# Kernel optimization log

Hardware: AMD Instinct MI355X
Metric: run time of the kernel (lower is better)

## Reference

```python
import jax, jax.numpy as jnp
import numpy as np

# Module hyperparameters (from init_kwargs)
N_HEAD = 16
D_K = 64
D_V = 64
TEMPERATURE = 0.7
TOP_K = 32
NEG_MIN = jnp.finfo(jnp.float32).min


def setup_inputs() -> dict:
    key = jax.random.key(0)
    ks = jax.random.split(key, 7)
    B, L, E = 2, 2048, 1024
    return {
        "q": jax.random.normal(ks[0], (B, L, E), jnp.float32),
        "k": jax.random.normal(ks[1], (B, L, E), jnp.float32),
        "v": jax.random.normal(ks[2], (B, L, D_V), jnp.float32),
        "w_q": jax.random.normal(ks[3], (N_HEAD * D_K, E), jnp.float32) * (E ** -0.5),
        "w_k": jax.random.normal(ks[4], (N_HEAD * D_K, E), jnp.float32) * (E ** -0.5),
        "w_v": jax.random.normal(ks[5], (N_HEAD * D_V, D_V), jnp.float32) * (D_V ** -0.5),
        "w_fc": jax.random.normal(ks[6], (D_V, N_HEAD * D_V), jnp.float32) * ((N_HEAD * D_V) ** -0.5),
    }


def _topk_restrict(logits):
    # Keep exactly TOP_K entries per row (scatter of top-k indices), fill rest with dtype min.
    B, H, Lq, Lk = logits.shape
    _, idx = jax.lax.top_k(logits, TOP_K)  # [B,H,Lq,TOP_K]
    bb = jnp.arange(B)[:, None, None, None]
    hh = jnp.arange(H)[None, :, None, None]
    qq = jnp.arange(Lq)[None, None, :, None]
    keep = jnp.zeros(logits.shape, bool).at[bb, hh, qq, idx].set(True)
    return jnp.where(keep, logits, NEG_MIN)


def reference(q, k, v, w_q, w_k, w_v, w_fc):
    B, Lq, _ = q.shape
    Lk = k.shape[1]
    Lv = v.shape[1]
    # Projections (bias-free linears), split heads: [B, H, L, d]
    q_proj = (q @ w_q.T).reshape(B, Lq, N_HEAD, D_K).transpose(0, 2, 1, 3)
    k_proj = (k @ w_k.T).reshape(B, Lk, N_HEAD, D_K).transpose(0, 2, 1, 3)
    v_proj = (v @ w_v.T).reshape(B, Lv, N_HEAD, D_V).transpose(0, 2, 1, 3)
    # Scaled QK^T in float32, then temperature scaling.
    logits = jnp.einsum("bhqd,bhkd->bhqk", q_proj / (D_K ** 0.5), k_proj).astype(jnp.float32)
    logits = logits / TEMPERATURE
    # Top-k restriction of attention logits (query_mask_flat=None -> applied to all queries).
    logits = _topk_restrict(logits)
    # Softmax selection; dropout is identity in eval / p=0.
    attn_probs = jax.nn.softmax(logits, axis=-1).astype(v.dtype)
    mixed = jnp.einsum("bhqk,bhkd->bhqd", attn_probs, v_proj)
    out = mixed.transpose(0, 2, 1, 3).reshape(B, Lq, N_HEAD * D_V)
    output = out @ w_fc.T
    return output, attn_probs
```

## Files before the change

### kernel.cpp

```cpp
#include <hip/hip_runtime.h>
#include <stdint.h>
#include <float.h>

constexpr int L = 2048;
constexpr int H = 16;
constexpr float SCALE = 0.17857142857142858f;
constexpr int OUT0 = 2 * 2048 * 64;
constexpr float QSTEP = 0.0625f;

typedef float f32x4 __attribute__((ext_vector_type(4)));
typedef short s16x8 __attribute__((ext_vector_type(8)));
typedef unsigned short u16x8 __attribute__((ext_vector_type(8)));
typedef _Float16 h16x8 __attribute__((ext_vector_type(8)));

__device__ __forceinline__ float wave_fmax(float x) {
#pragma unroll
  for (int s = 32; s; s >>= 1) x = fmaxf(x, __shfl_xor(x, s));
  return x;
}
__device__ __forceinline__ float wave_fsum(float x) {
#pragma unroll
  for (int s = 32; s; s >>= 1) x += __shfl_xor(x, s);
  return x;
}
__device__ __forceinline__ int wave_isum(int x) {
#pragma unroll
  for (int s = 32; s; s >>= 1) x += __shfl_xor(x, s);
  return x;
}
__device__ __forceinline__ unsigned f2sort(float f) {
  unsigned u = __float_as_uint(f);
  return (u & 0x80000000u) ? ~u : (u | 0x80000000u);
}
__device__ __forceinline__ void lds_fence() {
  __asm__ __volatile__("s_waitcnt lgkmcnt(0)" ::: "memory");
}

__device__ __forceinline__ void gload_lds16(const void* g, void* l) {
  __builtin_amdgcn_global_load_lds((const __attribute__((address_space(1))) void*)g,
                                   (__attribute__((address_space(3))) void*)l, 16, 0, 0);
}

__global__ __launch_bounds__(256) void split_kernel(
    const float* __restrict__ q, const float* __restrict__ k,
    const float* __restrict__ wq, const float* __restrict__ wk,
    unsigned short* __restrict__ qh, unsigned short* __restrict__ ql,
    unsigned short* __restrict__ kh, unsigned short* __restrict__ kl,
    unsigned short* __restrict__ wqh, unsigned short* __restrict__ wql,
    unsigned short* __restrict__ wkh, unsigned short* __restrict__ wkl) {
  const int y = blockIdx.y;
  const float* src = (y == 0) ? q : (y == 1) ? k : (y == 2) ? wq : wk;
  unsigned short* dh = (y == 0) ? qh : (y == 1) ? kh : (y == 2) ? wqh : wkh;
  unsigned short* dl = (y == 0) ? ql : (y == 1) ? kl : (y == 2) ? wql : wkl;
  const int n = (y < 2) ? (4096 * 1024) : (1024 * 1024);
  int idx = (blockIdx.x * 256 + threadIdx.x) * 4;
  const int stride = gridDim.x * 256 * 4;
  for (; idx < n; idx += stride) {
    float4 v = *(const float4*)(src + idx);
    float xs[4] = {v.x, v.y, v.z, v.w};
    unsigned short hs[4], ls[4];
#pragma unroll
    for (int i = 0; i < 4; ++i) {
      float x = xs[i] * 256.0f;
      _Float16 hh = (_Float16)x;
      float r = x - (float)hh;
      _Float16 ll = (_Float16)r;
      hs[i] = __builtin_bit_cast(unsigned short, hh);
      ls[i] = __builtin_bit_cast(unsigned short, ll);
    }
    *(ushort4*)(dh + idx) = make_ushort4(hs[0], hs[1], hs[2], hs[3]);
    *(ushort4*)(dl + idx) = make_ushort4(ls[0], ls[1], ls[2], ls[3]);
  }
}

__global__ __launch_bounds__(256, 2) void proj_split_kernel(
    const unsigned short* __restrict__ QH, const unsigned short* __restrict__ QL,
    const unsigned short* __restrict__ KH, const unsigned short* __restrict__ KL,
    const unsigned short* __restrict__ WQH, const unsigned short* __restrict__ WQL,
    const unsigned short* __restrict__ WKH, const unsigned short* __restrict__ WKL,
    float* __restrict__ QP, float* __restrict__ KP,
    unsigned short* __restrict__ Q16, unsigned short* __restrict__ K16) {
  __shared__ unsigned short sh[4][128 * 64];
  const int t = threadIdx.x;
  const int z = blockIdx.z;
  const int m0 = blockIdx.y * 128;
  const int n0 = blockIdx.x * 128;
  const unsigned short* xh = z ? KH : QH;
  const unsigned short* xl = z ? KL : QL;
  const unsigned short* wh = z ? WKH : WQH;
  const unsigned short* wl = z ? WKL : WQL;
  float* Y = z ? KP : QP;
  unsigned short* Y16 = z ? K16 : Q16;
  const unsigned short* mats[4] = {xh + (size_t)m0 * 1024, xl + (size_t)m0 * 1024,
                                   wh + (size_t)n0 * 1024, wl + (size_t)n0 * 1024};
  const int wv = t >> 6, lane = t & 63;
  const int wm = (wv & 1) * 64, wn = (wv >> 1) * 64;
  const int fr = lane & 15, quad = lane >> 4;
  f32x4 acc[16];
#pragma unroll
  for (int i = 0; i < 16; ++i) acc[i] = (f32x4){0.f, 0.f, 0.f, 0.f};

#define STAGE(cc)                                                              \
  {                                                                            \
    const int k0s = (cc) * 64;                                                 \
    _Pragma("unroll") for (int j = 0; j < 16; ++j) {                           \
      const int mat = j >> 2;                                                  \
      const int idx = (j & 3) * 256 + t;                                       \
      const int r = idx >> 3, p = idx & 7;                                     \
      const int sb = p ^ (r & 7);                                              \
      gload_lds16(mats[mat] + (size_t)r * 1024 + k0s + sb * 8, &sh[mat][idx * 8]); \
    }                                                                          \
  }

  STAGE(0);
  for (int c = 0; c < 16; ++c) {
    __syncthreads();
    h16x8 ah[2][4], alv[2][4], bh[2][4], blv[2][4];
#pragma unroll
    for (int kh2 = 0; kh2 < 2; ++kh2) {
#pragma unroll
      for (int mi = 0; mi < 4; ++mi) {
        int row = wm + mi * 16 + fr;
        int pp = (kh2 * 4 + quad) ^ (row & 7);
        ah[kh2][mi]  = *(const h16x8*)&sh[0][row * 64 + pp * 8];
        alv[kh2][mi] = *(const h16x8*)&sh[1][row * 64 + pp * 8];
      }
#pragma unroll
      for (int ni = 0; ni < 4; ++ni) {
        int row = wn + ni * 16 + fr;
        int pp = (kh2 * 4 + quad) ^ (row & 7);
        bh[kh2][ni]  = *(const h16x8*)&sh[2][row * 64 + pp * 8];
        blv[kh2][ni] = *(const h16x8*)&sh[3][row * 64 + pp * 8];
      }
    }
    __syncthreads();
    if (c < 15) STAGE(c + 1);
#pragma unroll
    for (int kh2 = 0; kh2 < 2; ++kh2)
#pragma unroll
      for (int mi = 0; mi < 4; ++mi)
#pragma unroll
        for (int ni = 0; ni < 4; ++ni) {
          acc[mi * 4 + ni] = __builtin_amdgcn_mfma_f32_16x16x32_f16(ah[kh2][mi], bh[kh2][ni], acc[mi * 4 + ni], 0, 0, 0);
          acc[mi * 4 + ni] = __builtin_amdgcn_mfma_f32_16x16x32_f16(ah[kh2][mi], blv[kh2][ni], acc[mi * 4 + ni], 0, 0, 0);
          acc[mi * 4 + ni] = __builtin_amdgcn_mfma_f32_16x16x32_f16(alv[kh2][mi], bh[kh2][ni], acc[mi * 4 + ni], 0, 0, 0);
        }
  }
#undef STAGE
#pragma unroll
  for (int mi = 0; mi < 4; ++mi)
#pragma unroll
    for (int ni = 0; ni < 4; ++ni) {
      int col = n0 + wn + ni * 16 + fr;
      int h = col >> 6, d = col & 63;
#pragma unroll
      for (int r = 0; r < 4; ++r) {
        int m = m0 + wm + mi * 16 + quad * 4 + r;
        int b = m >> 11, l = m & 2047;
        size_t off = (((size_t)b * H + h) * L + l) * 64 + d;
        float val = acc[mi * 4 + ni][r] * (1.0f / 65536.0f);
        Y[off] = val;
        _Float16 hf = (_Float16)val;
        Y16[off] = __builtin_bit_cast(unsigned short, hf);
      }
    }
}

template <int K, bool EMIT>
__global__ __launch_bounds__(256) void proj_kernel(const float* __restrict__ X,
                                                   const float* __restrict__ W,
                                                   float* __restrict__ Y,
                                                   unsigned short* __restrict__ Yb,
                                                   float bscale) {
  __shared__ float As[16][128];
  __shared__ float Bs[16][64];
  const int t = threadIdx.x;
  const int tx = t & 15;
  const int ty = t >> 4;
  const int m0 = blockIdx.y * 128;
  const int n0 = blockIdx.x * 64;
  const int ar = t >> 1, ac = (t & 1) * 8;
  const int br = t >> 2, bc = (t & 3) * 4;
  const float* xg = X + (size_t)(m0 + ar) * K + ac;
  const float* wg = W + (size_t)(n0 + br) * K + bc;
  float acc[8][4] = {};
  for (int k0 = 0; k0 < K; k0 += 16) {
    float4 a0 = *(const float4*)(xg + k0);
    float4 a1 = *(const float4*)(xg + k0 + 4);
    float4 b0 = *(const float4*)(wg + k0);
    __syncthreads();
    As[ac + 0][ar] = a0.x; As[ac + 1][ar] = a0.y; As[ac + 2][ar] = a0.z; As[ac + 3][ar] = a0.w;
    As[ac + 4][ar] = a1.x; As[ac + 5][ar] = a1.y; As[ac + 6][ar] = a1.z; As[ac + 7][ar] = a1.w;
    Bs[bc + 0][br] = b0.x; Bs[bc + 1][br] = b0.y; Bs[bc + 2][br] = b0.z; Bs[bc + 3][br] = b0.w;
    __syncthreads();
#pragma unroll
    for (int kk = 0; kk < 16; ++kk) {
      float4 av0 = *(const float4*)&As[kk][ty * 8];
      float4 av1 = *(const float4*)&As[kk][ty * 8 + 4];
      float4 bv = *(const float4*)&Bs[kk][tx * 4];
      float ar8[8] = {av0.x, av0.y, av0.z, av0.w, av1.x, av1.y, av1.z, av1.w};
      float br4[4] = {bv.x, bv.y, bv.z, bv.w};
#pragma unroll
      for (int i = 0; i < 8; ++i)
#pragma unroll
        for (int j = 0; j < 4; ++j) acc[i][j] = fmaf(ar8[i], br4[j], acc[i][j]);
    }
  }
  const int n = n0 + tx * 4;
  const int h = n >> 6, d = n & 63;
#pragma unroll
  for (int i = 0; i < 8; ++i) {
    int mm = m0 + ty * 8 + i;
    int b = mm >> 11, l = mm & 2047;
    size_t off = (((size_t)b * H + h) * L + l) * 64 + d;
    *(float4*)&Y[off] = make_float4(acc[i][0], acc[i][1], acc[i][2], acc[i][3]);
  }
}

constexpr int ALD = 72;
constexpr int CTB = 136;

__global__ __launch_bounds__(256) void alogits_kernel(const unsigned short* __restrict__ Qb,
                                                      const unsigned short* __restrict__ Kb,
                                                      char* __restrict__ AL) {
  __shared__ union {
    unsigned short qk[2][128 * ALD];
    char ct[128 * CTB];
  } sh;
  const int t = threadIdx.x;
  const int bh = blockIdx.z;
  const int m0 = blockIdx.y * 128, n0 = blockIdx.x * 128;
  const unsigned short* Qg = Qb + (size_t)bh * L * 64 + (size_t)m0 * 64;
  const unsigned short* Kg = Kb + (size_t)bh * L * 64 + (size_t)n0 * 64;
#pragma unroll
  for (int i = 0; i < 4; ++i) {
    int blk = t * 4 + i;
    int r = blk >> 3, lb = blk & 7;
    *(u16x8*)&sh.qk[0][r * ALD + lb * 8] = *(const u16x8*)&Qg[r * 64 + lb * 8];
    *(u16x8*)&sh.qk[1][r * ALD + lb * 8] = *(const u16x8*)&Kg[r * 64 + lb * 8];
  }
  __syncthreads();
  const int wv = t >> 6, lane = t & 63;
  const int wm = (wv & 1) * 64, wn = (wv >> 1) * 64;
  const int fr = lane & 15, quad = lane >> 4;
  f32x4 acc[16];
#pragma unroll
  for (int i = 0; i < 16; ++i) acc[i] = (f32x4){0.f, 0.f, 0.f, 0.f};
#pragma unroll
  for (int kh = 0; kh < 2; ++kh) {
    h16x8 a[4], b[4];
#pragma unroll
    for (int mi = 0; mi < 4; ++mi)
      a[mi] = *(const h16x8*)&sh.qk[0][(wm + mi * 16 + fr) * ALD + kh * 32 + quad * 8];
#pragma unroll
    for (int ni = 0; ni < 4; ++ni)
      b[ni] = *(const h16x8*)&sh.qk[1][(wn + ni * 16 + fr) * ALD + kh * 32 + quad * 8];
#pragma unroll
    for (int mi = 0; mi < 4; ++mi)
#pragma unroll
      for (int ni = 0; ni < 4; ++ni)
        acc[mi * 4 + ni] = __builtin_amdgcn_mfma_f32_16x16x32_f16(
            a[mi], b[ni], acc[mi * 4 + ni], 0, 0, 0);
  }
  __syncthreads();
#pragma unroll
  for (int mi = 0; mi < 4; ++mi)
#pragma unroll
    for (int ni = 0; ni < 4; ++ni) {
      int col = wn + ni * 16 + fr;
#pragma unroll
      for (int r = 0; r < 4; ++r) {
        int rowl = wm + mi * 16 + quad * 4 + r;
        float sc = acc[mi * 4 + ni][r] * 2.8571428571428572f;
        sc = fminf(fmaxf(sc, -127.0f), 127.0f);
        sh.ct[rowl * CTB + col] = (char)__float2int_rn(sc);
      }
    }
  __syncthreads();
  char* Abase = AL + (size_t)bh * L * L;
  const int rq = lane >> 4;
  const int cq = (lane & 15) * 8;
#pragma unroll
  for (int it = 0; it < 8; ++it) {
    int row = wv * 32 + it * 4 + rq;
    uint2 v8 = *(const uint2*)&sh.ct[row * CTB + cq];
    __builtin_nontemporal_store(v8.x, (unsigned*)&Abase[(size_t)(m0 + row) * L + n0 + cq]);
    __builtin_nontemporal_store(v8.y, (unsigned*)&Abase[(size_t)(m0 + row) * L + n0 + cq + 4]);
  }
}

__global__ __launch_bounds__(256) void select_kernel(const char* __restrict__ AL,
                                                     const float* __restrict__ Qp,
                                                     const float* __restrict__ Kp,
                                                     const float* __restrict__ Vp,
                                                     float* __restrict__ Probs,
                                                     float* __restrict__ Mixed) {
  __shared__ float prow[4][2048];
  __shared__ float qbuf[4][64];
  __shared__ float cbuf[4][64];
  __shared__ int ibufc[4][64];
  __shared__ float pbuf[4][32];
  __shared__ int ibuf[4][32];
  const int lane = threadIdx.x & 63;
  const int w = threadIdx.x >> 6;
  const int row = blockIdx.x * 4 + w;
  const int bh = row >> 11;
  const int q = row & 2047;
  const unsigned long long below = (lane == 63) ? 0x7fffffffffffffffull
                                                : ((1ull << lane) - 1ull);
  const unsigned* Arow = (const unsigned*)(AL + (size_t)row * 2048);

  float lg[32];
#pragma unroll
  for (int u2 = 0; u2 < 8; ++u2) {
    unsigned dw = __builtin_nontemporal_load(Arow + u2 * 64 + lane);
#pragma unroll
    for (int b = 0; b < 4; ++b)
      lg[u2 * 4 + b] = (float)((char)(dw >> (8 * b))) * QSTEP;
  }
#pragma unroll
  for (int u = 0; u < 32; ++u) prow[w][u * 64 + lane] = 0.f;
  if (lane < 16)
    *(float4*)&qbuf[w][lane * 4] = *(const float4*)&Qp[((size_t)bh * L + q) * 64 + lane * 4];

  float m = lg[0];
#pragma unroll
  for (int u = 1; u < 32; ++u) m = fmaxf(m, lg[u]);
  m = wave_fmax(m);

  float T = 0.f;
  bool found = false;
  float cut = m - 2.2f;
  float lo = 0.f, hi = m;
  bool has_lo = false;
  for (int attempt = 0; attempt < 8 && !found; ++attempt) {
    int c = 0;
#pragma unroll
    for (int u = 0; u < 32; ++u) c += (lg[u] > cut) ? 1 : 0;
    c = wave_isum(c);
    if (c < 32) {
      hi = cut;
      cut = has_lo ? 0.5f * (lo + cut) : (cut - 0.45f);
    } else if (c > 64) {
      lo = cut; has_lo = true;
      cut = 0.5f * (cut + hi);
    } else {
      int base = 0;
#pragma unroll
      for (int u = 0; u < 32; ++u) {
        bool cd = lg[u] > cut;
        unsigned long long mk = __ballot(cd);
        if (cd) cbuf[w][base + __popcll(mk & below)] = lg[u];
        base += __popcll(mk);
      }
      lds_fence();
      float v2 = (lane < c) ? cbuf[w][lane] : -FLT_MAX;
#pragma unroll
      for (int size = 2; size <= 64; size <<= 1)
#pragma unroll
        for (int stride = size >> 1; stride; stride >>= 1) {
          float pv = __shfl_xor(v2, stride);
          bool lower = (lane & stride) == 0;
          bool asc = (lane & size) == 0;
          v2 = (lower == asc) ? fminf(v2, pv) : fmaxf(v2, pv);
        }
      T = __shfl(v2, 32);
      found = true;
    }
  }
  if (!found) {
    unsigned tb = 0;
    for (int bit = 31; bit >= 0; --bit) {
      unsigned cand = tb | (1u << bit);
      int c = 0;
#pragma unroll
      for (int u = 0; u < 32; ++u) c += (f2sort(lg[u]) >= cand) ? 1 : 0;
      c = wave_isum(c);
      if (c >= 32) tb = cand;
    }
    T = (tb & 0x80000000u) ? __uint_as_float(tb & 0x7fffffffu) : __uint_as_float(~tb);
  }

  float theta = T;
  int c2 = 0;
  const float margs[5] = {0.40f, 0.25f, 0.15f, 0.08f, 0.0f};
#pragma unroll
  for (int a = 0; a < 5; ++a) {
    float th = T - margs[a];
    int c = 0;
#pragma unroll
    for (int u = 0; u < 32; ++u) c += (lg[u] >= th) ? 1 : 0;
    c = wave_isum(c);
    theta = th; c2 = c;
    if (c <= 64) break;
  }
  if (c2 > 64) c2 = 64;

  {
    int base = 0;
#pragma unroll
    for (int u = 0; u < 32; ++u) {
      bool cd = lg[u] >= theta;
      unsigned long long mk = __ballot(cd);
      if (cd) {
        int s = base + __popcll(mk & below);
        if (s < 64) ibufc[w][s] = ((u >> 2) * 64 + lane) * 4 + (u & 3);
      }
      base += __popcll(mk);
    }
  }
  lds_fence();

  int myi = (lane < c2) ? ibufc[w][lane] : 0x7fffffff;
  float vex = -FLT_MAX;
  if (lane < c2) {
    const float4* K4 = (const float4*)(Kp + ((size_t)bh * L + myi) * 64);
    const float4* Q4 = (const float4*)&qbuf[w][0];
    float acc = 0.f;
#pragma unroll
    for (int dq = 0; dq < 16; ++dq) {
      float4 kv = K4[dq];
      float4 qv = Q4[dq];
      acc = fmaf(qv.x, kv.x, acc);
      acc = fmaf(qv.y, kv.y, acc);
      acc = fmaf(qv.z, kv.z, acc);
      acc = fmaf(qv.w, kv.w, acc);
    }
    vex = (acc * 0.125f) / 0.7f;
  }

  unsigned long long key = ((unsigned long long)(~f2sort(vex)) << 32) | (unsigned)myi;
#pragma unroll
  for (int size = 2; size <= 64; size <<= 1)
#pragma unroll
    for (int stride = size >> 1; stride; stride >>= 1) {
      unsigned long long pk = __shfl_xor(key, stride);
      unsigned long long mn = key < pk ? key : pk;
      unsigned long long mx = key < pk ? pk : key;
      bool keepmin = ((lane & stride) == 0) == ((lane & size) == 0);
      key = keepmin ? mn : mx;
    }
  unsigned uv = ~(unsigned)(key >> 32);
  float vs = __uint_as_float((uv & 0x80000000u) ? (uv & 0x7fffffffu) : ~uv);
  int sidx = (int)(unsigned)(key & 0xffffffffull);

  float vmax = __shfl(vs, 0);
  float e = (lane < 32) ? __expf(vs - vmax) : 0.f;
  float S = wave_fsum(e);
  float p = e / S;
  if (lane < 32) {
    pbuf[w][lane] = p;
    ibuf[w][lane] = sidx;
    prow[w][sidx] = p;
  }
  lds_fence();

  float* Prow = Probs + (size_t)row * 2048;
#pragma unroll
  for (int u = 0; u < 32; ++u)
    __builtin_nontemporal_store(prow[w][u * 64 + lane], Prow + u * 64 + lane);

  const float* Vb = Vp + (size_t)bh * L * 64;
  float accv = 0.f;
#pragma unroll
  for (int i = 0; i < 32; ++i)
    accv = fmaf(pbuf[w][i], Vb[(size_t)ibuf[w][i] * 64 + lane], accv);
  const int bb = bh >> 4, hh = bh & 15;
  Mixed[((size_t)(bb * 2048 + q)) * 1024 + hh * 64 + lane] = accv;
}

__global__ __launch_bounds__(256) void fc_kernel(const float* __restrict__ Mx,
                                                 const float* __restrict__ Wfc,
                                                 float* __restrict__ Out) {
  __shared__ float As[32][64];
  __shared__ float Ws[64][64];
  const int t = threadIdx.x;
  const int tx = t & 15;
  const int ty = t >> 4;
  const int m0 = blockIdx.x * 32;
  float acc[2][4] = {};
  for (int k0 = 0; k0 < 1024; k0 += 64) {
    __syncthreads();
    {
      int lin = t * 8;
      int rr = lin >> 6, kk = lin & 63;
      *(float4*)&As[rr][kk] = *(const float4*)&Mx[(size_t)(m0 + rr) * 1024 + k0 + kk];
      *(float4*)&As[rr][kk + 4] = *(const float4*)&Mx[(size_t)(m0 + rr) * 1024 + k0 + kk + 4];
    }
    {
      int n = t >> 2;
      int kq = (t & 3) * 16;
#pragma unroll
      for (int u = 0; u < 4; ++u) {
        float4 wv = *(const float4*)&Wfc[(size_t)n * 1024 + k0 + kq + u * 4];
        Ws[kq + u * 4 + 0][n] = wv.x;
        Ws[kq + u * 4 + 1][n] = wv.y;
        Ws[kq + u * 4 + 2][n] = wv.z;
        Ws[kq + u * 4 + 3][n] = wv.w;
      }
    }
    __syncthreads();
#pragma unroll
    for (int kk = 0; kk < 64; ++kk) {
      float a0 = As[ty][kk], a1 = As[ty + 16][kk];
      float4 wv = *(const float4*)&Ws[kk][tx * 4];
      float wr[4] = {wv.x, wv.y, wv.z, wv.w};
#pragma unroll
      for (int j = 0; j < 4; ++j) {
        acc[0][j] = fmaf(a0, wr[j], acc[0][j]);
        acc[1][j] = fmaf(a1, wr[j], acc[1][j]);
      }
    }
  }
#pragma unroll
  for (int i = 0; i < 2; ++i) {
    int mm = m0 + ty + i * 16;
    *(float4*)&Out[(size_t)mm * 64 + tx * 4] =
        make_float4(acc[i][0], acc[i][1], acc[i][2], acc[i][3]);
  }
}

extern "C" void kernel_launch(void* const* d_in, const int* in_sizes, int n_in,
                              void* d_out, int out_size, void* d_ws, size_t ws_size,
                              hipStream_t stream) {
  const float* q    = (const float*)d_in[0];
  const float* k    = (const float*)d_in[1];
  const float* v    = (const float*)d_in[2];
  const float* w_q  = (const float*)d_in[3];
  const float* w_k  = (const float*)d_in[4];
  const float* w_v  = (const float*)d_in[5];
  const float* w_fc = (const float*)d_in[6];

  float* out = (float*)d_out;
  float* probs = out + OUT0;

  float* ws = (float*)d_ws;
  float* q_proj = ws;
  float* k_proj = ws + 4194304;
  float* v_proj = ws + 8388608;
  float* mixed  = ws + 12582912;
  unsigned short* qb = (unsigned short*)(ws + 16777216);
  unsigned short* kb = (unsigned short*)(ws + 18874368);
  char* al = (char*)(ws + 20971520);

  unsigned short* qh  = (unsigned short*)((char*)d_ws + 234881024);
  unsigned short* ql  = qh + 4194304;
  unsigned short* kh  = ql + 4194304;
  unsigned short* kl  = kh + 4194304;
  unsigned short* wqh = kl + 4194304;
  unsigned short* wql = wqh + 1048576;
  unsigned short* wkh = wql + 1048576;
  unsigned short* wkl = wkh + 1048576;

  dim3 blk(256);
  split_kernel<<<dim3(1024, 4), blk, 0, stream>>>(q, k, w_q, w_k,
                                                  qh, ql, kh, kl, wqh, wql, wkh, wkl);
  proj_split_kernel<<<dim3(8, 32, 2), blk, 0, stream>>>(qh, ql, kh, kl,
                                                        wqh, wql, wkh, wkl,
                                                        q_proj, k_proj, qb, kb);
  proj_kernel<64, false><<<dim3(16, 32), blk, 0, stream>>>(v, w_v, v_proj, nullptr, 1.0f);
  alogits_kernel<<<dim3(16, 16, 32), blk, 0, stream>>>(qb, kb, al);
  select_kernel<<<dim3(16384), blk, 0, stream>>>(al, q_proj, k_proj, v_proj, probs, mixed);
  fc_kernel<<<dim3(128), blk, 0, stream>>>(mixed, w_fc, out);
}
```

Before: 862.7 us.

## Replace float threshold search and bitonic sorts with integer bisection and radix select

The select kernel now keeps the int8-quantized logits as integers and finds the top-32 threshold by an 8-step integer bisection. This replaces the adaptive float cut search, the candidate bitonic sort and the 32-step fallback. The final top-32 selection over exact scores uses a ballot-based bitwise radix select with index tie-breaking instead of a 64-bit bitonic sort. Wave reductions move from shuffles to DPP row operations with readlane. This cuts shuffle and sort work per row, at the cost of more intricate tie handling and reliance on DPP semantics.

```diff
diff --git a/kernel.cpp b/kernel.cpp
--- a/kernel.cpp
+++ b/kernel.cpp
@@ -13,27 +13,57 @@
 typedef unsigned short u16x8 __attribute__((ext_vector_type(8)));
 typedef _Float16 h16x8 __attribute__((ext_vector_type(8)));
 
-__device__ __forceinline__ float wave_fmax(float x) {
-#pragma unroll
-  for (int s = 32; s; s >>= 1) x = fmaxf(x, __shfl_xor(x, s));
-  return x;
-}
-__device__ __forceinline__ float wave_fsum(float x) {
-#pragma unroll
-  for (int s = 32; s; s >>= 1) x += __shfl_xor(x, s);
-  return x;
-}
-__device__ __forceinline__ int wave_isum(int x) {
-#pragma unroll
-  for (int s = 32; s; s >>= 1) x += __shfl_xor(x, s);
-  return x;
-}
 __device__ __forceinline__ unsigned f2sort(float f) {
   unsigned u = __float_as_uint(f);
   return (u & 0x80000000u) ? ~u : (u | 0x80000000u);
 }
 __device__ __forceinline__ void lds_fence() {
   __asm__ __volatile__("s_waitcnt lgkmcnt(0)" ::: "memory");
+}
+
+__device__ __forceinline__ int wave_isum_dpp(int x) {
+#define DPP_ADDI(CTRL) x += __builtin_amdgcn_update_dpp(0, x, CTRL, 0xf, 0xf, true);
+  DPP_ADDI(0x111) DPP_ADDI(0x112) DPP_ADDI(0x114)
+  DPP_ADDI(0x118) DPP_ADDI(0x142) DPP_ADDI(0x143)
+#undef DPP_ADDI
+  return __builtin_amdgcn_readlane(x, 63);
+}
+__device__ __forceinline__ float wave_fsum_dpp(float x) {
+  int xi = __builtin_bit_cast(int, x);
+#define DPP_ADDF(CTRL)                                                      \
+  {                                                                         \
+    int _s = __builtin_amdgcn_update_dpp(0, xi, CTRL, 0xf, 0xf, true);      \
+    x = x + __builtin_bit_cast(float, _s);                                  \
+    xi = __builtin_bit_cast(int, x);                                        \
+  }
+  DPP_ADDF(0x111) DPP_ADDF(0x112) DPP_ADDF(0x114)
+  DPP_ADDF(0x118) DPP_ADDF(0x142) DPP_ADDF(0x143)
+#undef DPP_ADDF
+  return __builtin_bit_cast(float, __builtin_amdgcn_readlane(xi, 63));
+}
+__device__ __forceinline__ float wave_fmax_dpp(float x) {
+  int xi = __builtin_bit_cast(int, x);
+#define DPP_MAXF(CTRL)                                                      \
+  {                                                                         \
+    int _s = __builtin_amdgcn_update_dpp(xi, xi, CTRL, 0xf, 0xf, false);    \
+    x = fmaxf(x, __builtin_bit_cast(float, _s));                            \
+    xi = __builtin_bit_cast(int, x);                                        \
+  }
+  DPP_MAXF(0x111) DPP_MAXF(0x112) DPP_MAXF(0x114)
+  DPP_MAXF(0x118) DPP_MAXF(0x142) DPP_MAXF(0x143)
+#undef DPP_MAXF
+  return __builtin_bit_cast(float, __builtin_amdgcn_readlane(xi, 63));
+}
+__device__ __forceinline__ int wave_imin_dpp(int x) {
+#define DPP_MINI(CTRL)                                                      \
+  {                                                                         \
+    int _s = __builtin_amdgcn_update_dpp(x, x, CTRL, 0xf, 0xf, false);      \
+    x = min(x, _s);                                                         \
+  }
+  DPP_MINI(0x111) DPP_MINI(0x112) DPP_MINI(0x114)
+  DPP_MINI(0x118) DPP_MINI(0x142) DPP_MINI(0x143)
+#undef DPP_MINI
+  return __builtin_amdgcn_readlane(x, 63);
 }
 
 __device__ __forceinline__ void gload_lds16(const void* g, void* l) {
@@ -297,7 +327,6 @@
                                                      float* __restrict__ Mixed) {
   __shared__ float prow[4][2048];
   __shared__ float qbuf[4][64];
-  __shared__ float cbuf[4][64];
   __shared__ int ibufc[4][64];
   __shared__ float pbuf[4][32];
   __shared__ int ibuf[4][32];
@@ -310,87 +339,41 @@
                                                 : ((1ull << lane) - 1ull);
   const unsigned* Arow = (const unsigned*)(AL + (size_t)row * 2048);
 
-  float lg[32];
+  int li[32];
 #pragma unroll
   for (int u2 = 0; u2 < 8; ++u2) {
     unsigned dw = __builtin_nontemporal_load(Arow + u2 * 64 + lane);
 #pragma unroll
     for (int b = 0; b < 4; ++b)
-      lg[u2 * 4 + b] = (float)((char)(dw >> (8 * b))) * QSTEP;
+      li[u2 * 4 + b] = (int)((char)(dw >> (8 * b)));
   }
 #pragma unroll
   for (int u = 0; u < 32; ++u) prow[w][u * 64 + lane] = 0.f;
   if (lane < 16)
     *(float4*)&qbuf[w][lane * 4] = *(const float4*)&Qp[((size_t)bh * L + q) * 64 + lane * 4];
 
-  float m = lg[0];
-#pragma unroll
-  for (int u = 1; u < 32; ++u) m = fmaxf(m, lg[u]);
-  m = wave_fmax(m);
-
-  float T = 0.f;
-  bool found = false;
-  float cut = m - 2.2f;
-  float lo = 0.f, hi = m;
-  bool has_lo = false;
-  for (int attempt = 0; attempt < 8 && !found; ++attempt) {
+  int tlo = -128, thi = 128;
+#pragma unroll
+  for (int it = 0; it < 8; ++it) {
+    int mid = (tlo + thi) >> 1;
     int c = 0;
 #pragma unroll
-    for (int u = 0; u < 32; ++u) c += (lg[u] > cut) ? 1 : 0;
-    c = wave_isum(c);
-    if (c < 32) {
-      hi = cut;
-      cut = has_lo ? 0.5f * (lo + cut) : (cut - 0.45f);
-    } else if (c > 64) {
-      lo = cut; has_lo = true;
-      cut = 0.5f * (cut + hi);
-    } else {
-      int base = 0;
-#pragma unroll
-      for (int u = 0; u < 32; ++u) {
-        bool cd = lg[u] > cut;
-        unsigned long long mk = __ballot(cd);
-        if (cd) cbuf[w][base + __popcll(mk & below)] = lg[u];
-        base += __popcll(mk);
-      }
-      lds_fence();
-      float v2 = (lane < c) ? cbuf[w][lane] : -FLT_MAX;
-#pragma unroll
-      for (int size = 2; size <= 64; size <<= 1)
-#pragma unroll
-        for (int stride = size >> 1; stride; stride >>= 1) {
-          float pv = __shfl_xor(v2, stride);
-          bool lower = (lane & stride) == 0;
-          bool asc = (lane & size) == 0;
-          v2 = (lower == asc) ? fminf(v2, pv) : fmaxf(v2, pv);
-        }
-      T = __shfl(v2, 32);
-      found = true;
-    }
-  }
-  if (!found) {
-    unsigned tb = 0;
-    for (int bit = 31; bit >= 0; --bit) {
-      unsigned cand = tb | (1u << bit);
-      int c = 0;
-#pragma unroll
-      for (int u = 0; u < 32; ++u) c += (f2sort(lg[u]) >= cand) ? 1 : 0;
-      c = wave_isum(c);
-      if (c >= 32) tb = cand;
-    }
-    T = (tb & 0x80000000u) ? __uint_as_float(tb & 0x7fffffffu) : __uint_as_float(~tb);
-  }
-
-  float theta = T;
+    for (int u = 0; u < 32; ++u) c += (li[u] >= mid) ? 1 : 0;
+    c = wave_isum_dpp(c);
+    if (c >= 32) tlo = mid; else thi = mid;
+  }
+  const int t32 = tlo;
+
+  int theta = t32;
   int c2 = 0;
-  const float margs[5] = {0.40f, 0.25f, 0.15f, 0.08f, 0.0f};
+  const int margs[5] = {6, 4, 2, 1, 0};
 #pragma unroll
   for (int a = 0; a < 5; ++a) {
-    float th = T - margs[a];
+    int th = t32 - margs[a];
     int c = 0;
 #pragma unroll
-    for (int u = 0; u < 32; ++u) c += (lg[u] >= th) ? 1 : 0;
-    c = wave_isum(c);
+    for (int u = 0; u < 32; ++u) c += (li[u] >= th) ? 1 : 0;
+    c = wave_isum_dpp(c);
     theta = th; c2 = c;
     if (c <= 64) break;
   }
@@ -400,7 +383,7 @@
     int base = 0;
 #pragma unroll
     for (int u = 0; u < 32; ++u) {
-      bool cd = lg[u] >= theta;
+      bool cd = li[u] >= theta;
       unsigned long long mk = __ballot(cd);
       if (cd) {
         int s = base + __popcll(mk & below);
@@ -429,29 +412,42 @@
     vex = (acc * 0.125f) / 0.7f;
   }
 
-  unsigned long long key = ((unsigned long long)(~f2sort(vex)) << 32) | (unsigned)myi;
-#pragma unroll
-  for (int size = 2; size <= 64; size <<= 1)
-#pragma unroll
-    for (int stride = size >> 1; stride; stride >>= 1) {
-      unsigned long long pk = __shfl_xor(key, stride);
-      unsigned long long mn = key < pk ? key : pk;
-      unsigned long long mx = key < pk ? pk : key;
-      bool keepmin = ((lane & stride) == 0) == ((lane & size) == 0);
-      key = keepmin ? mn : mx;
-    }
-  unsigned uv = ~(unsigned)(key >> 32);
-  float vs = __uint_as_float((uv & 0x80000000u) ? (uv & 0x7fffffffu) : ~uv);
-  int sidx = (int)(unsigned)(key & 0xffffffffull);
-
-  float vmax = __shfl(vs, 0);
-  float e = (lane < 32) ? __expf(vs - vmax) : 0.f;
-  float S = wave_fsum(e);
+  const unsigned sk = f2sort(vex);
+  unsigned tb = 0;
+#pragma unroll
+  for (int bit = 31; bit >= 0; --bit) {
+    unsigned cand = tb | (1u << bit);
+    int cnt = (int)__popcll(__ballot(sk >= cand));
+    if (cnt >= 32) tb = cand;
+  }
+  bool kept = sk > tb;
+  {
+    int cnt_gt = (int)__popcll(__ballot(kept));
+    int need = 32 - cnt_gt;
+    unsigned long long tiem = __ballot(sk == tb);
+    if ((int)__popcll(tiem) <= need) {
+      kept = kept || (sk == tb);
+    } else {
+      bool isT = (sk == tb);
+      for (int r = 0; r < need; ++r) {
+        int mi = wave_imin_dpp(isT ? myi : 0x7fffffff);
+        if (isT && myi == mi) { kept = true; isT = false; }
+      }
+    }
+  }
+
+  float vmax = wave_fmax_dpp(vex);
+  float e = kept ? __expf(vex - vmax) : 0.f;
+  float S = wave_fsum_dpp(e);
   float p = e / S;
-  if (lane < 32) {
-    pbuf[w][lane] = p;
-    ibuf[w][lane] = sidx;
-    prow[w][sidx] = p;
+  {
+    unsigned long long km = __ballot(kept);
+    int slot = (int)__popcll(km & below);
+    if (kept) {
+      pbuf[w][slot] = p;
+      ibuf[w][slot] = myi;
+      prow[w][myi] = p;
+    }
   }
   lds_fence();
 
```

Measured after the change: 855.2 us. No clear change (-0.9%).
